# Kernel optimization log

Measured on AMD Instinct MI355X. Metric: run time of the kernel, lower is better.

The kernel has to match this reference:

```python
import jax, jax.numpy as jnp
import numpy as np

TAU = 2.0        # LIFNode default tau
V_TH = 1.0       # v_threshold
BN_EPS = 1e-5


def setup_inputs() -> dict:
    key = jax.random.key(0)
    k1, k2 = jax.random.split(key)
    T, B, C, V, E = 16, 512, 2, 25, 256
    x = jax.random.normal(k1, (T, B, C, V), dtype=jnp.float32)
    W = jax.random.normal(k2, (E, C), dtype=jnp.float32) * 0.5  # conv1x1 weight [out,in]
    gamma = jnp.ones((E,), dtype=jnp.float32)
    beta = jnp.zeros((E,), dtype=jnp.float32)
    return {"x": x, "W": W, "gamma": gamma, "beta": beta}


def reference(x, W, gamma, beta):
    # x: [T, B, C, V]; conv1d(k=1) == channel-mixing matmul
    y = jnp.einsum('tbcv,ec->tbev', x, W)  # [T, B, E, V]
    # BatchNorm1d in training mode: stats over (T*B, V) per channel
    mean = jnp.mean(y, axis=(0, 1, 3), keepdims=True)
    var = jnp.var(y, axis=(0, 1, 3), keepdims=True)
    y = (y - mean) * jax.lax.rsqrt(var + BN_EPS)
    y = y * gamma[None, None, :, None] + beta[None, None, :, None]
    # Multi-step LIF: v += (x - (v - v_reset))/tau; spike = v >= v_th; hard reset to v_reset=0
    v0 = jnp.zeros(y.shape[1:], dtype=y.dtype)  # [B, E, V]
    def step(v, xt):
        v = v + (xt - v) / TAU
        spike = (v >= V_TH).astype(v.dtype)
        v = v * (1.0 - spike)  # hard reset, v_reset = 0
        return v, spike
    _, spikes = jax.lax.scan(step, v0, y)
    return spikes  # [T, B, E, V]
```

## Files before the change

kernel.cpp:

```cpp
#include <hip/hip_runtime.h>
#include <math.h>

constexpr int T = 16, B = 512, C = 2, V = 25, E = 256;
constexpr int EV  = E * V;
constexpr int BEV = B * EV;
constexpr int XT  = B * C * V;
constexpr int NB  = 1600;
constexpr int CHUNKS = 25;
constexpr int BPC = 64;
constexpr int NROWS = 7;
constexpr float NF = 204800.0f;

#define WS_M32(ws) ((float*)(ws))
#define WS_R32(ws) ((float*)(ws) + E)

template<int PASS>
__global__ void __launch_bounds__(256) k_bs(const float* __restrict__ x,
                                            const float* __restrict__ W,
                                            const float* __restrict__ ws,
                                            float* __restrict__ bs) {
    __shared__ float sx[NROWS * 50];
    int p  = blockIdx.x;
    int q0 = p * 128;
    int row_lo = q0 / 25;
    for (int i = threadIdx.x; i < NROWS * 50; i += 256) {
        int r = i / 50;
        if (row_lo + r < 8192) sx[i] = x[(row_lo + r) * 50 + (i - r * 50)];
    }
    __syncthreads();

    int e = threadIdx.x;
    float w0 = W[e * 2 + 0];
    float w1 = W[e * 2 + 1];
    float mn = (PASS == 1) ? WS_M32(ws)[e] : 0.0f;

    int v   = q0 - row_lo * 25;
    int off = v;
    float r[8];
    #pragma unroll
    for (int k = 0; k < 128; k++) {
        float y = __fadd_rn(__fmul_rn(w0, sx[off]), __fmul_rn(w1, sx[off + 25]));
        if (PASS == 1) {
            float d = __fsub_rn(y, mn);
            y = __fmul_rn(d, d);
        }
        int j = k & 7;
        r[j] = (k < 8) ? y : __fadd_rn(r[j], y);
        v++; off++;
        if (v == 25) { v = 0; off += 25; }
    }
    bs[p * 256 + e] =
        __fadd_rn(__fadd_rn(__fadd_rn(r[0], r[1]), __fadd_rn(r[2], r[3])),
                  __fadd_rn(__fadd_rn(r[4], r[5]), __fadd_rn(r[6], r[7])));
}

template<int WHICH>
__global__ void __launch_bounds__(64) k_comb(const float* __restrict__ bs,
                                             float* __restrict__ ws) {
    __shared__ float cb[NB];
    __shared__ float csum[CHUNKS];
    int e = blockIdx.x;
    for (int i = threadIdx.x; i < NB; i += 64) cb[i] = bs[i * 256 + e];
    __syncthreads();
    if (threadIdx.x < CHUNKS) {
        int c = threadIdx.x;
        float t[BPC];
        #pragma unroll
        for (int i = 0; i < BPC; i++) t[i] = cb[c * BPC + i];
        #pragma unroll
        for (int m = BPC / 2; m >= 1; m >>= 1) {
            #pragma unroll
            for (int i = 0; i < m; i++)
                t[i] = __fadd_rn(t[2 * i], t[2 * i + 1]);
        }
        csum[c] = t[0];
    }
    __syncthreads();
    if (threadIdx.x == 0) {
        float acc = 0.0f;
        #pragma unroll
        for (int c = 0; c < CHUNKS; c++) acc = __fadd_rn(acc, csum[c]);
        if (WHICH == 0) {
            WS_M32(ws)[e] = __fdiv_rn(acc, NF);
        } else {
            float var = __fdiv_rn(acc, NF);
            WS_R32(ws)[e] = __fdiv_rn(1.0f, __fsqrt_rn(__fadd_rn(var, 1e-5f)));
        }
    }
}

__global__ void __launch_bounds__(256) k_main(const float* __restrict__ x,
                                              const float* __restrict__ W,
                                              const float* __restrict__ g,
                                              const float* __restrict__ bb,
                                              const float* __restrict__ ws,
                                              float* __restrict__ out) {
    __shared__ float sx[T * 50];
    int blk = blockIdx.x;
    int b   = blk / 25;
    int seg = blk - b * 25;
    for (int i = threadIdx.x; i < T * 50; i += 256) {
        int t = i / 50;
        sx[i] = x[b * 50 + t * XT + (i - t * 50)];
    }
    __syncthreads();

    int idx = blk * 256 + threadIdx.x;
    int rem = seg * 256 + threadIdx.x;
    int e   = rem / V;
    int v   = rem - e * V;
    float w0 = W[e * 2 + 0];
    float w1 = W[e * 2 + 1];
    float mn = WS_M32(ws)[e];
    float rs = WS_R32(ws)[e];
    float ga = g[e];
    float be = bb[e];
    float vm = 0.0f;
    #pragma unroll
    for (int t = 0; t < T; t++) {
        float x0 = sx[t * 50 + v];
        float x1 = sx[t * 50 + 25 + v];
        float y = __fadd_rn(__fmul_rn(w0, x0), __fmul_rn(w1, x1));
        y = __fmul_rn(__fsub_rn(y, mn), rs);
        y = __fadd_rn(__fmul_rn(y, ga), be);
        float d = __fmul_rn(__fsub_rn(y, vm), 0.5f);
        vm = __fadd_rn(vm, d);
        bool sp = (vm >= 1.0f);
        __builtin_nontemporal_store(sp ? 1.0f : 0.0f,
                                    &out[(size_t)t * BEV + idx]);
        if (sp) vm = 0.0f;
    }
}

extern "C" void kernel_launch(void* const* d_in, const int* in_sizes, int n_in,
                              void* d_out, int out_size, void* d_ws, size_t ws_size,
                              hipStream_t stream) {
    (void)in_sizes; (void)n_in; (void)out_size; (void)ws_size;
    const float* x  = (const float*)d_in[0];
    const float* W  = (const float*)d_in[1];
    const float* g  = (const float*)d_in[2];
    const float* bb = (const float*)d_in[3];
    float* ws = (float*)d_ws;
    float* bs = (float*)d_out;

    k_bs<0><<<NB, 256, 0, stream>>>(x, W, ws, bs);
    k_comb<0><<<E, 64, 0, stream>>>(bs, ws);
    k_bs<1><<<NB, 256, 0, stream>>>(x, W, ws, bs);
    k_comb<1><<<E, 64, 0, stream>>>(bs, ws);
    k_main<<<BEV / 256, 256, 0, stream>>>(x, W, g, bb, ws, (float*)d_out);
}
```

Before: 259.5 us.

## Vectorize main kernel output to float4 stores, widen comb blocks

```diff
diff --git a/kernel.cpp b/kernel.cpp
--- a/kernel.cpp
+++ b/kernel.cpp
@@ -10,6 +10,8 @@
 constexpr int BPC = 64;
 constexpr int NROWS = 7;
 constexpr float NF = 204800.0f;
+
+typedef float f32x4 __attribute__((ext_vector_type(4)));
 
 #define WS_M32(ws) ((float*)(ws))
 #define WS_R32(ws) ((float*)(ws) + E)
@@ -55,12 +57,12 @@
 }
 
 template<int WHICH>
-__global__ void __launch_bounds__(64) k_comb(const float* __restrict__ bs,
-                                             float* __restrict__ ws) {
+__global__ void __launch_bounds__(256) k_comb(const float* __restrict__ bs,
+                                              float* __restrict__ ws) {
     __shared__ float cb[NB];
     __shared__ float csum[CHUNKS];
     int e = blockIdx.x;
-    for (int i = threadIdx.x; i < NB; i += 64) cb[i] = bs[i * 256 + e];
+    for (int i = threadIdx.x; i < NB; i += 256) cb[i] = bs[i * 256 + e];
     __syncthreads();
     if (threadIdx.x < CHUNKS) {
         int c = threadIdx.x;
@@ -92,43 +94,67 @@
 __global__ void __launch_bounds__(256) k_main(const float* __restrict__ x,
                                               const float* __restrict__ W,
                                               const float* __restrict__ g,
-                                              const float* __restrict__ bb,
+                                              const float* __restrict__ bta,
                                               const float* __restrict__ ws,
                                               float* __restrict__ out) {
-    __shared__ float sx[T * 50];
+    __shared__ float sx[2 * T * 50];
     int blk = blockIdx.x;
-    int b   = blk / 25;
-    int seg = blk - b * 25;
-    for (int i = threadIdx.x; i < T * 50; i += 256) {
-        int t = i / 50;
-        sx[i] = x[b * 50 + t * XT + (i - t * 50)];
+    int gi0 = blk * 1024;
+    int b0  = gi0 / EV;
+    int nb  = ((gi0 + 1023) / EV == b0) ? 1 : 2;
+    for (int i = threadIdx.x; i < nb * 800; i += 256) {
+        int bi  = i / 800;
+        int r   = i - bi * 800;
+        int tt  = r / 50;
+        sx[i] = x[(b0 + bi) * 50 + tt * XT + (r - tt * 50)];
     }
     __syncthreads();
 
-    int idx = blk * 256 + threadIdx.x;
-    int rem = seg * 256 + threadIdx.x;
-    int e   = rem / V;
-    int v   = rem - e * V;
-    float w0 = W[e * 2 + 0];
-    float w1 = W[e * 2 + 1];
-    float mn = WS_M32(ws)[e];
-    float rs = WS_R32(ws)[e];
-    float ga = g[e];
-    float be = bb[e];
-    float vm = 0.0f;
+    int gi  = gi0 + threadIdx.x * 4;
+    int b   = gi / EV;
+    int rem = gi - b * EV;
+    int e0  = rem / V;
+    int v0  = rem - e0 * V;
+    int sb  = (b - b0) * 800;
+    int e1  = (e0 < E - 1) ? e0 + 1 : e0;
+    float w00 = W[e0 * 2], w01 = W[e0 * 2 + 1];
+    float w10 = W[e1 * 2], w11 = W[e1 * 2 + 1];
+    float mn0 = WS_M32(ws)[e0], mn1 = WS_M32(ws)[e1];
+    float rs0 = WS_R32(ws)[e0], rs1 = WS_R32(ws)[e1];
+    float ga0 = g[e0],  ga1 = g[e1];
+    float be0 = bta[e0], be1 = bta[e1];
+
+    float wA[4], wB[4], mn[4], rs[4], ga[4], be[4];
+    int   vv[4];
+    #pragma unroll
+    for (int j = 0; j < 4; j++) {
+        int  vj = v0 + j;
+        bool cr = (vj >= V);
+        vv[j] = cr ? vj - V : vj;
+        wA[j] = cr ? w10 : w00;  wB[j] = cr ? w11 : w01;
+        mn[j] = cr ? mn1 : mn0;  rs[j] = cr ? rs1 : rs0;
+        ga[j] = cr ? ga1 : ga0;  be[j] = cr ? be1 : be0;
+    }
+
+    float vm[4] = {0.0f, 0.0f, 0.0f, 0.0f};
     #pragma unroll
     for (int t = 0; t < T; t++) {
-        float x0 = sx[t * 50 + v];
-        float x1 = sx[t * 50 + 25 + v];
-        float y = __fadd_rn(__fmul_rn(w0, x0), __fmul_rn(w1, x1));
-        y = __fmul_rn(__fsub_rn(y, mn), rs);
-        y = __fadd_rn(__fmul_rn(y, ga), be);
-        float d = __fmul_rn(__fsub_rn(y, vm), 0.5f);
-        vm = __fadd_rn(vm, d);
-        bool sp = (vm >= 1.0f);
-        __builtin_nontemporal_store(sp ? 1.0f : 0.0f,
-                                    &out[(size_t)t * BEV + idx]);
-        if (sp) vm = 0.0f;
+        f32x4 o;
+        #pragma unroll
+        for (int j = 0; j < 4; j++) {
+            float x0 = sx[sb + t * 50 + vv[j]];
+            float x1 = sx[sb + t * 50 + 25 + vv[j]];
+            float y = __fadd_rn(__fmul_rn(wA[j], x0), __fmul_rn(wB[j], x1));
+            y = __fmul_rn(__fsub_rn(y, mn[j]), rs[j]);
+            y = __fadd_rn(__fmul_rn(y, ga[j]), be[j]);
+            float d = __fmul_rn(__fsub_rn(y, vm[j]), 0.5f);
+            vm[j] = __fadd_rn(vm[j], d);
+            bool sp = (vm[j] >= 1.0f);
+            o[j] = sp ? 1.0f : 0.0f;
+            if (sp) vm[j] = 0.0f;
+        }
+        __builtin_nontemporal_store(o,
+            reinterpret_cast<f32x4*>(&out[(size_t)t * BEV + gi]));
     }
 }
 
@@ -144,8 +170,8 @@
     float* bs = (float*)d_out;
 
     k_bs<0><<<NB, 256, 0, stream>>>(x, W, ws, bs);
-    k_comb<0><<<E, 64, 0, stream>>>(bs, ws);
+    k_comb<0><<<E, 256, 0, stream>>>(bs, ws);
     k_bs<1><<<NB, 256, 0, stream>>>(x, W, ws, bs);
-    k_comb<1><<<E, 64, 0, stream>>>(bs, ws);
-    k_main<<<BEV / 256, 256, 0, stream>>>(x, W, g, bb, ws, (float*)d_out);
+    k_comb<1><<<E, 256, 0, stream>>>(bs, ws);
+    k_main<<<BEV / 1024, 256, 0, stream>>>(x, W, g, bb, ws, (float*)d_out);
 }
```

New measurement: 259.8 us. About the same (+0.1%).
